# Kernel tuning notes

Hardware: AMD Instinct MI355X
Metric: run time of the kernel (lower is better)

## Reference

```python
import jax, jax.numpy as jnp
import numpy as np

DIM = 1024
NUM_HEADS = 16
HEAD_DIM = DIM // NUM_HEADS           # 64
WIDTH_SCALE = 0.5                      # set via configure_width in the source
CUR_HD = int(HEAD_DIM * WIDTH_SCALE)   # 32
CUR_DIM = CUR_HD * NUM_HEADS           # 512
SCALE = (HEAD_DIM ** -0.5) / (WIDTH_SCALE ** 0.5)
B, N = 2, 2048


def setup_inputs() -> dict:
    key = jax.random.key(0)
    k1, k2, k3 = jax.random.split(key, 3)
    x = jax.random.normal(k1, (B, N, DIM), dtype=jnp.float32)
    # 0.02 init keeps pre-softmax logits in a realistic range
    w_qkv = jax.random.normal(k2, (3 * DIM, DIM), dtype=jnp.float32) * 0.02
    w_proj = jax.random.normal(k3, (DIM, DIM), dtype=jnp.float32) * 0.02
    b_proj = jnp.zeros((DIM,), dtype=jnp.float32)
    return {"x": x, "w_qkv": w_qkv, "w_proj": w_proj, "b_proj": b_proj}


def reference(x, w_qkv, w_proj, b_proj):
    Bb, Nn, C = x.shape
    cq = 3 * CUR_DIM
    # dynamic-width slice of the fused QKV weight (qkv_bias=False)
    qkv = x @ w_qkv[:cq, :].T                              # (B, N, 3*CUR_DIM)
    qkv = qkv.reshape(Bb, Nn, 3, NUM_HEADS, CUR_HD).transpose(2, 0, 3, 1, 4)
    q, k, v = qkv[0], qkv[1], qkv[2]                       # (B, H, N, hd)
    attn = jax.nn.softmax(jnp.einsum('bhnd,bhmd->bhnm', q, k) * SCALE, axis=-1)
    o = jnp.einsum('bhnm,bhmd->bhnd', attn, v)             # (B, H, N, hd)
    o = o.transpose(0, 2, 1, 3).reshape(Bb, Nn, CUR_DIM)
    # proj uses only its first CUR_DIM input columns
    return o @ w_proj[:, :CUR_DIM].T + b_proj
```

## Files before the change

### kernel.cpp

```cpp
#include <hip/hip_runtime.h>

typedef __bf16 bf16;
typedef __bf16 bf16x8 __attribute__((ext_vector_type(8)));
typedef __bf16 bf16x4 __attribute__((ext_vector_type(4)));
typedef __bf16 bf16x2 __attribute__((ext_vector_type(2)));
typedef float  f32x4  __attribute__((ext_vector_type(4)));
typedef float  f32x16 __attribute__((ext_vector_type(16)));
typedef unsigned int uint32;

constexpr int DIM_  = 1024;
constexpr int NH    = 16;
constexpr int CHD   = 32;
constexpr int CDIM  = 512;
constexpr int CQ    = 1536;
constexpr int NSEQ  = 2048;
constexpr int M_    = 4096;
constexpr float ATT_SCALE = 0.17677669529663687f;
constexpr float QS_LOG2 = ATT_SCALE * 1.4426950408889634f;

__device__ inline void gload16(const bf16* g, bf16* l) {
    __builtin_amdgcn_global_load_lds((const __attribute__((address_space(1))) void*)g,
                                     (__attribute__((address_space(3))) void*)l, 16, 0, 0);
}

constexpr int NX4 = M_ * DIM_ / 4;
constexpr int NW4 = CQ * DIM_ / 4;
constexpr int NP4 = DIM_ * (CDIM / 4);
__global__ void cast_fused(const float* __restrict__ x, const float* __restrict__ wq,
                           const float* __restrict__ wp, bf16* __restrict__ xb,
                           bf16* __restrict__ wqb, bf16* __restrict__ wpb) {
    int i = blockIdx.x * blockDim.x + threadIdx.x;
    const float4* src;
    bf16x4* dst;
    if (i < NX4) {
        src = reinterpret_cast<const float4*>(x) + i;
        dst = reinterpret_cast<bf16x4*>(xb) + i;
    } else if (i < NX4 + NW4) {
        int j = i - NX4;
        src = reinterpret_cast<const float4*>(wq) + j;
        dst = reinterpret_cast<bf16x4*>(wqb) + j;
    } else {
        int j = i - (NX4 + NW4);
        int c = j >> 7, j4 = j & 127;
        src = reinterpret_cast<const float4*>(wp + c * DIM_) + j4;
        dst = reinterpret_cast<bf16x4*>(wpb + c * CDIM) + j4;
    }
    float4 v = *src;
    bf16x4 o = { (bf16)v.x, (bf16)v.y, (bf16)v.z, (bf16)v.w };
    *dst = o;
}

template<int KDIM, int MODE>
__launch_bounds__(256)
__global__ void gemm_nt(const bf16* __restrict__ A, const bf16* __restrict__ Bm,
                        bf16* __restrict__ qbo, bf16* __restrict__ kbo, bf16* __restrict__ vto,
                        float* __restrict__ Cf, const float* __restrict__ bias) {
    __shared__ __align__(16) bf16 SMEM[24576];
    bf16* As = SMEM;
    bf16* Bs = SMEM + 16384;
    const int tid = threadIdx.x;
    const int w = tid >> 6, lane = tid & 63;
    const int m0 = blockIdx.x * 128, n0 = blockIdx.y * 64;
    const int wr = (w >> 1) * 64, wc = (w & 1) * 32;
    const int cl = lane & 15, hi = lane >> 4;
    const int swz = cl & 7;

    const int srow = lane >> 3, schk = (lane & 7) ^ (lane >> 3);
    const bf16* gaA = A  + (m0 + srow) * KDIM + schk * 8;
    const bf16* gbB = Bm + (n0 + srow) * KDIM + schk * 8;

    constexpr int KT = KDIM / 64;

    auto stage = [&](int kt, int b) {
#pragma unroll
        for (int i = 0; i < 4; ++i)
            gload16(gaA + (w * 4 + i) * 8 * KDIM + kt * 64, As + b * 8192 + (w * 4 + i) * 512);
#pragma unroll
        for (int i = 0; i < 2; ++i)
            gload16(gbB + (w * 2 + i) * 8 * KDIM + kt * 64, Bs + b * 4096 + (w * 2 + i) * 512);
    };
    stage(0, 0);
    __syncthreads();

    f32x4 acc[4][2] = {};

    for (int kt = 0; kt < KT; ++kt) {
        if (kt + 1 < KT) stage(kt + 1, (kt + 1) & 1);
        const bf16* as = As + (kt & 1) * 8192;
        const bf16* bs = Bs + (kt & 1) * 4096;
#pragma unroll
        for (int kh = 0; kh < 2; ++kh) {
            const int ck = ((kh * 4 + hi) ^ swz) * 8;
            bf16x8 af[4], bfr[2];
#pragma unroll
            for (int i = 0; i < 4; ++i)
                af[i]  = *reinterpret_cast<const bf16x8*>(as + (wr + i * 16 + cl) * 64 + ck);
#pragma unroll
            for (int j = 0; j < 2; ++j)
                bfr[j] = *reinterpret_cast<const bf16x8*>(bs + (wc + j * 16 + cl) * 64 + ck);
#pragma unroll
            for (int i = 0; i < 4; ++i)
#pragma unroll
                for (int j = 0; j < 2; ++j)
                    acc[i][j] = __builtin_amdgcn_mfma_f32_16x16x32_bf16(af[i], bfr[j], acc[i][j], 0, 0, 0);
        }
        __syncthreads();
    }

    const int rg = hi * 4;
    if constexpr (MODE == 2) {
#pragma unroll
        for (int i = 0; i < 4; ++i)
#pragma unroll
            for (int j = 0; j < 2; ++j) {
                const int row = m0 + wr + i * 16 + rg;
                const int col = n0 + wc + j * 16 + cl;
                const float bv = bias[col];
#pragma unroll
                for (int r = 0; r < 4; ++r)
                    Cf[(row + r) * DIM_ + col] = acc[i][j][r] + bv;
            }
    } else {
        const int sec = n0 >> 9;
        if (sec == 2) {
#pragma unroll
            for (int i = 0; i < 4; ++i)
#pragma unroll
                for (int j = 0; j < 2; ++j) {
                    const int row = m0 + wr + i * 16 + rg;
                    const int col = n0 + wc + j * 16 + cl;
                    const int rem = col & 511;
                    const int h = rem >> 5, d = rem & 31;
                    const int bb = row >> 11, pos = row & 2047;
                    const int bh = bb * NH + h;
                    bf16x4 st;
#pragma unroll
                    for (int r = 0; r < 4; ++r) st[r] = (bf16)acc[i][j][r];
                    *reinterpret_cast<bf16x4*>(vto + (bh * CHD + d) * NSEQ + pos) = st;
                }
        } else {
            const float sc = sec ? 1.0f : QS_LOG2;
            __syncthreads();
#pragma unroll
            for (int i = 0; i < 4; ++i)
#pragma unroll
                for (int j = 0; j < 2; ++j)
#pragma unroll
                    for (int r = 0; r < 4; ++r)
                        SMEM[(wr + i * 16 + rg + r) * 72 + wc + j * 16 + cl] =
                            (bf16)(acc[i][j][r] * sc);
            __syncthreads();
            const int row = tid >> 1, ch = (tid & 1) * 32;
            const int m = m0 + row, bb = m >> 11, pos = m & 2047;
            const int col0 = n0 + ch;
            const int h = (col0 & 511) >> 5;
            bf16* dst = (sec ? kbo : qbo) + ((bb * NH + h) * NSEQ + pos) * CHD;
#pragma unroll
            for (int v4 = 0; v4 < 4; ++v4)
                *reinterpret_cast<bf16x8*>(dst + v4 * 8) =
                    *reinterpret_cast<const bf16x8*>(SMEM + row * 72 + ch + v4 * 8);
        }
    }
}

__device__ inline uint32 pkbf(float lo, float hi) {
    bf16x2 t = { (bf16)lo, (bf16)hi };
    return __builtin_bit_cast(uint32, t);
}

__launch_bounds__(1024, 8)
__global__ void flash_kernel(const bf16* __restrict__ qb, const bf16* __restrict__ kb,
                             const bf16* __restrict__ vt, bf16* __restrict__ outb) {
    __shared__ __align__(16) char smem[65536];
    const int tid = threadIdx.x;
    const int w = tid >> 6, lane = tid & 63;
    const int lq = lane & 31, hi = lane >> 5;
    const int p = w & 3, qt = w >> 2;

    const int blin = blockIdx.x;
    const int xcd = blin & 7, within = blin >> 3;
    const int head = xcd * 4 + (within >> 4);
    const int qblk = within & 15;
    const int q0 = qblk * 128 + p * 32;

    const bf16* Q = qb + head * (NSEQ * CHD);
    const bf16* K = kb + head * (NSEQ * CHD);
    const bf16* V = vt + head * (CHD * NSEQ);

    const bf16x8 qf0 = *reinterpret_cast<const bf16x8*>(Q + (q0 + lq) * CHD + hi * 8);
    const bf16x8 qf1 = *reinterpret_cast<const bf16x8*>(Q + (q0 + lq) * CHD + 16 + hi * 8);

    char* base = smem + qt * 16384;
    const int kvbeg = qt * 512;
    const int sh = p >> 1, skc = p & 1;
    const bf16* srcK = K + (kvbeg + sh * 32 + lq) * CHD + skc * 16 + hi * 8;
    const bf16* srcV = V + lq * NSEQ + kvbeg + p * 16 + hi * 8;

    auto stage = [&](int t) {
        char* b = base + (t & 1) * 8192;
        gload16(srcK + t * 64 * CHD, (bf16*)(b + p * 1024));
        gload16(srcV + t * 64,       (bf16*)(b + 4096 + p * 1024));
    };
    stage(0);
    __syncthreads();

    f32x16 o = {};
    float rs[4] = {};
    const f32x16 zero16 = {};

    for (int t = 0; t < 8; ++t) {
        if (t < 7) stage(t + 1);
        char* buf = base + (t & 1) * 8192;
#pragma unroll
        for (int h = 0; h < 2; ++h) {
            const bf16x8 k0 = *reinterpret_cast<const bf16x8*>(buf + (h * 2 + 0) * 1024 + lane * 16);
            const bf16x8 k1 = *reinterpret_cast<const bf16x8*>(buf + (h * 2 + 1) * 1024 + lane * 16);
            __builtin_amdgcn_s_setprio(1);
            f32x16 s = __builtin_amdgcn_mfma_f32_32x32x16_bf16(k0, qf0, zero16, 0, 0, 0);
            s = __builtin_amdgcn_mfma_f32_32x32x16_bf16(k1, qf1, s, 0, 0, 0);
            __builtin_amdgcn_s_setprio(0);

#pragma unroll
            for (int r = 0; r < 16; ++r) s[r] = __builtin_amdgcn_exp2f(s[r]);
#pragma unroll
            for (int r = 0; r < 16; ++r) rs[r & 3] += s[r];

#pragma unroll
            for (int cc = 0; cc < 2; ++cc) {
                const int b8 = cc * 8;
                uint32 u0 = pkbf(s[b8 + 0], s[b8 + 1]);
                uint32 u1 = pkbf(s[b8 + 2], s[b8 + 3]);
                uint32 u2 = pkbf(s[b8 + 4], s[b8 + 5]);
                uint32 u3 = pkbf(s[b8 + 6], s[b8 + 7]);
                asm volatile("v_permlane32_swap_b32 %0, %1" : "+v"(u0), "+v"(u2));
                asm volatile("v_permlane32_swap_b32 %0, %1" : "+v"(u1), "+v"(u3));
                union { uint32 u[4]; bf16x8 v; } pb;
                pb.u[0] = u0; pb.u[1] = u1; pb.u[2] = u2; pb.u[3] = u3;
                const bf16x8 vf = *reinterpret_cast<const bf16x8*>(buf + 4096 + (h * 2 + cc) * 1024 + lane * 16);
                __builtin_amdgcn_s_setprio(1);
                o = __builtin_amdgcn_mfma_f32_32x32x16_bf16(vf, pb.v, o, 0, 0, 0);
                __builtin_amdgcn_s_setprio(0);
            }
        }
        __syncthreads();
    }

    float ls = (rs[0] + rs[1]) + (rs[2] + rs[3]);
    ls += __shfl_xor(ls, 32);

    if (qt) {
        float* Mo = (float*)(smem + p * 13824 + (qt - 1) * 4608);
        float* Ml = (float*)(smem + p * 13824 + (qt - 1) * 4608 + 4096);
#pragma unroll
        for (int r = 0; r < 16; ++r) Mo[r * 64 + lane] = o[r];
        Ml[lane] = ls;
    }
    __syncthreads();
    if (!qt) {
        float lt = ls;
        f32x16 ot = o;
#pragma unroll
        for (int q = 0; q < 3; ++q) {
            const float* Mo = (const float*)(smem + p * 13824 + q * 4608);
            const float* Ml = (const float*)(smem + p * 13824 + q * 4608 + 4096);
            lt += Ml[lane];
#pragma unroll
            for (int r = 0; r < 16; ++r) ot[r] += Mo[r * 64 + lane];
        }
        const float inv = 1.f / lt;
        const int bb = head >> 4, hh = head & 15;
        const int row = bb * NSEQ + q0 + lq;
        const int colb = hh * CHD;
#pragma unroll
        for (int rq = 0; rq < 4; ++rq) {
            bf16x4 st;
#pragma unroll
            for (int ri = 0; ri < 4; ++ri)
                st[ri] = (bf16)(ot[rq * 4 + ri] * inv);
            *reinterpret_cast<bf16x4*>(outb + row * CDIM + colb + rq * 8 + hi * 4) = st;
        }
    }
}

extern "C" void kernel_launch(void* const* d_in, const int* in_sizes, int n_in,
                              void* d_out, int out_size, void* d_ws, size_t ws_size,
                              hipStream_t stream) {
    const float* x      = (const float*)d_in[0];
    const float* w_qkv  = (const float*)d_in[1];
    const float* w_proj = (const float*)d_in[2];
    const float* b_proj = (const float*)d_in[3];
    float* out = (float*)d_out;

    char* ws = (char*)d_ws;
    bf16* xb  = (bf16*)(ws);
    bf16* wqb = (bf16*)(ws + 8388608);
    bf16* wpb = (bf16*)(ws + 11534336);
    bf16* qb  = (bf16*)(ws + 25165824);
    bf16* kb  = (bf16*)(ws + 29360128);
    bf16* vt  = (bf16*)(ws + 33554432);
    bf16* ob  = (bf16*)(ws + 37748736);

    cast_fused<<<(NX4 + NW4 + NP4) / 256, 256, 0, stream>>>(x, w_qkv, w_proj, xb, wqb, wpb);

    gemm_nt<DIM_, 1><<<dim3(32, 24), 256, 0, stream>>>(xb, wqb, qb, kb, vt, nullptr, nullptr);

    flash_kernel<<<512, 1024, 0, stream>>>(qb, kb, vt, ob);

    gemm_nt<CDIM, 2><<<dim3(32, 16), 256, 0, stream>>>(ob, wpb, nullptr, nullptr, nullptr, out, b_proj);
}
```

Measured before the change: 68.17 us.

## Split flash attention KV range across two wave groups instead of four

The flash kernel now uses 512 threads per block, with 2 wave groups each covering half of the KV sequence (1024 keys) instead of 4 groups covering 512 each. Each stage loads 128 keys per tile with double buffering, which halves the cross-group reduction of partial outputs through shared memory. The exp2 is also interleaved per 8-element chunk with packing, which may lower register pressure. In exchange each wave runs a longer serial loop and there are fewer waves per block to hide latency.

```diff
diff --git a/kernel.cpp b/kernel.cpp
--- a/kernel.cpp
+++ b/kernel.cpp
@@ -168,14 +168,14 @@
     return __builtin_bit_cast(uint32, t);
 }
 
-__launch_bounds__(1024, 8)
+__launch_bounds__(512, 4)
 __global__ void flash_kernel(const bf16* __restrict__ qb, const bf16* __restrict__ kb,
                              const bf16* __restrict__ vt, bf16* __restrict__ outb) {
     __shared__ __align__(16) char smem[65536];
     const int tid = threadIdx.x;
     const int w = tid >> 6, lane = tid & 63;
     const int lq = lane & 31, hi = lane >> 5;
-    const int p = w & 3, qt = w >> 2;
+    const int p = w & 3, half = w >> 2;
 
     const int blin = blockIdx.x;
     const int xcd = blin & 7, within = blin >> 3;
@@ -190,16 +190,16 @@
     const bf16x8 qf0 = *reinterpret_cast<const bf16x8*>(Q + (q0 + lq) * CHD + hi * 8);
     const bf16x8 qf1 = *reinterpret_cast<const bf16x8*>(Q + (q0 + lq) * CHD + 16 + hi * 8);
 
-    char* base = smem + qt * 16384;
-    const int kvbeg = qt * 512;
-    const int sh = p >> 1, skc = p & 1;
-    const bf16* srcK = K + (kvbeg + sh * 32 + lq) * CHD + skc * 16 + hi * 8;
-    const bf16* srcV = V + lq * NSEQ + kvbeg + p * 16 + hi * 8;
+    char* base = smem + half * 32768;
+    const bf16* srcK = K + (half * 1024 + p * 32 + lq) * CHD + hi * 8;
+    const bf16* srcV = V + lq * NSEQ + half * 1024 + p * 32 + hi * 8;
 
     auto stage = [&](int t) {
-        char* b = base + (t & 1) * 8192;
-        gload16(srcK + t * 64 * CHD, (bf16*)(b + p * 1024));
-        gload16(srcV + t * 64,       (bf16*)(b + 4096 + p * 1024));
+        char* b = base + (t & 1) * 16384;
+        gload16(srcK + t * 128 * CHD,      (bf16*)(b + (2 * p) * 1024));
+        gload16(srcK + t * 128 * CHD + 16, (bf16*)(b + (2 * p + 1) * 1024));
+        gload16(srcV + t * 128,            (bf16*)(b + 8192 + (2 * p) * 1024));
+        gload16(srcV + t * 128 + 16,       (bf16*)(b + 8192 + (2 * p + 1) * 1024));
     };
     stage(0);
     __syncthreads();
@@ -210,33 +210,33 @@
 
     for (int t = 0; t < 8; ++t) {
         if (t < 7) stage(t + 1);
-        char* buf = base + (t & 1) * 8192;
-#pragma unroll
-        for (int h = 0; h < 2; ++h) {
-            const bf16x8 k0 = *reinterpret_cast<const bf16x8*>(buf + (h * 2 + 0) * 1024 + lane * 16);
-            const bf16x8 k1 = *reinterpret_cast<const bf16x8*>(buf + (h * 2 + 1) * 1024 + lane * 16);
+        char* buf = base + (t & 1) * 16384;
+#pragma unroll
+        for (int h = 0; h < 4; ++h) {
+            const bf16x8 k0 = *reinterpret_cast<const bf16x8*>(buf + (2 * h) * 1024 + lane * 16);
+            const bf16x8 k1 = *reinterpret_cast<const bf16x8*>(buf + (2 * h + 1) * 1024 + lane * 16);
             __builtin_amdgcn_s_setprio(1);
             f32x16 s = __builtin_amdgcn_mfma_f32_32x32x16_bf16(k0, qf0, zero16, 0, 0, 0);
             s = __builtin_amdgcn_mfma_f32_32x32x16_bf16(k1, qf1, s, 0, 0, 0);
             __builtin_amdgcn_s_setprio(0);
 
 #pragma unroll
-            for (int r = 0; r < 16; ++r) s[r] = __builtin_amdgcn_exp2f(s[r]);
-#pragma unroll
-            for (int r = 0; r < 16; ++r) rs[r & 3] += s[r];
-
-#pragma unroll
             for (int cc = 0; cc < 2; ++cc) {
                 const int b8 = cc * 8;
-                uint32 u0 = pkbf(s[b8 + 0], s[b8 + 1]);
-                uint32 u1 = pkbf(s[b8 + 2], s[b8 + 3]);
-                uint32 u2 = pkbf(s[b8 + 4], s[b8 + 5]);
-                uint32 u3 = pkbf(s[b8 + 6], s[b8 + 7]);
+                float e[8];
+#pragma unroll
+                for (int j = 0; j < 8; ++j) e[j] = __builtin_amdgcn_exp2f(s[b8 + j]);
+#pragma unroll
+                for (int j = 0; j < 8; ++j) rs[j & 3] += e[j];
+                uint32 u0 = pkbf(e[0], e[1]);
+                uint32 u1 = pkbf(e[2], e[3]);
+                uint32 u2 = pkbf(e[4], e[5]);
+                uint32 u3 = pkbf(e[6], e[7]);
                 asm volatile("v_permlane32_swap_b32 %0, %1" : "+v"(u0), "+v"(u2));
                 asm volatile("v_permlane32_swap_b32 %0, %1" : "+v"(u1), "+v"(u3));
                 union { uint32 u[4]; bf16x8 v; } pb;
                 pb.u[0] = u0; pb.u[1] = u1; pb.u[2] = u2; pb.u[3] = u3;
-                const bf16x8 vf = *reinterpret_cast<const bf16x8*>(buf + 4096 + (h * 2 + cc) * 1024 + lane * 16);
+                const bf16x8 vf = *reinterpret_cast<const bf16x8*>(buf + 8192 + (2 * h + cc) * 1024 + lane * 16);
                 __builtin_amdgcn_s_setprio(1);
                 o = __builtin_amdgcn_mfma_f32_32x32x16_bf16(vf, pb.v, o, 0, 0, 0);
                 __builtin_amdgcn_s_setprio(0);
@@ -248,26 +248,16 @@
     float ls = (rs[0] + rs[1]) + (rs[2] + rs[3]);
     ls += __shfl_xor(ls, 32);
 
-    if (qt) {
-        float* Mo = (float*)(smem + p * 13824 + (qt - 1) * 4608);
-        float* Ml = (float*)(smem + p * 13824 + (qt - 1) * 4608 + 4096);
+    float* Mo = (float*)(smem + p * 4608);
+    float* Ml = (float*)(smem + p * 4608 + 4096);
+    if (half) {
 #pragma unroll
         for (int r = 0; r < 16; ++r) Mo[r * 64 + lane] = o[r];
         Ml[lane] = ls;
     }
     __syncthreads();
-    if (!qt) {
-        float lt = ls;
-        f32x16 ot = o;
-#pragma unroll
-        for (int q = 0; q < 3; ++q) {
-            const float* Mo = (const float*)(smem + p * 13824 + q * 4608);
-            const float* Ml = (const float*)(smem + p * 13824 + q * 4608 + 4096);
-            lt += Ml[lane];
-#pragma unroll
-            for (int r = 0; r < 16; ++r) ot[r] += Mo[r * 64 + lane];
-        }
-        const float inv = 1.f / lt;
+    if (!half) {
+        const float inv = 1.f / (ls + Ml[lane]);
         const int bb = head >> 4, hh = head & 15;
         const int row = bb * NSEQ + q0 + lq;
         const int colb = hh * CHD;
@@ -276,7 +266,7 @@
             bf16x4 st;
 #pragma unroll
             for (int ri = 0; ri < 4; ++ri)
-                st[ri] = (bf16)(ot[rq * 4 + ri] * inv);
+                st[ri] = (bf16)((o[rq * 4 + ri] + Mo[(rq * 4 + ri) * 64 + lane]) * inv);
             *reinterpret_cast<bf16x4*>(outb + row * CDIM + colb + rq * 8 + hi * 4) = st;
         }
     }
@@ -304,7 +294,7 @@
 
     gemm_nt<DIM_, 1><<<dim3(32, 24), 256, 0, stream>>>(xb, wqb, qb, kb, vt, nullptr, nullptr);
 
-    flash_kernel<<<512, 1024, 0, stream>>>(qb, kb, vt, ob);
+    flash_kernel<<<512, 512, 0, stream>>>(qb, kb, vt, ob);
 
     gemm_nt<CDIM, 2><<<dim3(32, 16), 256, 0, stream>>>(ob, wpb, nullptr, nullptr, nullptr, out, b_proj);
 }
```

After: 68.70 us. Within noise of the previous version (+0.8%).
